# Optimization experiments

Hardware: AMD Instinct MI355X
Metric: run time of the kernel (lower is better)

The kernel has to match this reference:

```python
import jax, jax.numpy as jnp
import numpy as np

SEQ, BATCH, IN_DIM, HID_DIM = 512, 256, 256, 256
NQ = 8
ALPHA = 0.5
MLP_HID = 128


def _linear_init(key, fan_in, fan_out):
    k1, k2 = jax.random.split(key)
    bound = 1.0 / np.sqrt(fan_in)
    W = jax.random.uniform(k1, (fan_in, fan_out), minval=-bound, maxval=bound, dtype=jnp.float32)
    b = jax.random.uniform(k2, (fan_out,), minval=-bound, maxval=bound, dtype=jnp.float32)
    return W, b


def setup_inputs() -> dict:
    key = jax.random.key(0)
    ks = jax.random.split(key, 12)
    cdim = IN_DIM + HID_DIM
    inputs = jax.random.normal(ks[0], (SEQ, BATCH, IN_DIM), dtype=jnp.float32)
    W1, b1 = _linear_init(ks[1], cdim, MLP_HID)
    W2, b2 = _linear_init(ks[2], MLP_HID, NQ * 4)
    Wf, bf = _linear_init(ks[3], cdim, 1)
    Wi, bi = _linear_init(ks[4], cdim, 1)
    Wg, bg = _linear_init(ks[5], cdim, 1)
    Wo, bo = _linear_init(ks[6], cdim, 1)
    rzf = jax.random.normal(ks[7], (NQ,), dtype=jnp.float32)
    rzi = jax.random.normal(ks[8], (NQ,), dtype=jnp.float32)
    rzg = jax.random.normal(ks[9], (NQ,), dtype=jnp.float32)
    rzo = jax.random.normal(ks[10], (NQ,), dtype=jnp.float32)
    return dict(inputs=inputs, W1=W1, b1=b1, W2=W2, b2=b2,
                Wf=Wf, bf=bf, Wi=Wi, bi=bi, Wg=Wg, bg=bg, Wo=Wo, bo=bo,
                rzf=rzf, rzi=rzi, rzg=rzg, rzo=rzo)


def _qgate(theta):
    # Analytic expectations of the RX/RZ/CNOT-chain circuit:
    # <Z_k> = prod_{j<=k} cos(theta_j); rz_params cancel in Z expectations.
    # Returns mean over wires, shape (batch, 1).
    return jnp.mean(jnp.cumprod(jnp.cos(theta), axis=-1), axis=-1, keepdims=True)


def reference(inputs, W1, b1, W2, b2, Wf, bf, Wi, bi, Wg, bg, Wo, bo, rzf, rzi, rzg, rzo):
    batch = inputs.shape[1]
    hx0 = jnp.zeros((batch, HID_DIM), dtype=inputs.dtype)
    cx0 = jnp.zeros((batch, HID_DIM), dtype=inputs.dtype)

    def step(carry, x):
        hx, cx = carry
        combined = jnp.concatenate([x, hx], axis=1)  # (B, in+hid)
        f_c = jax.nn.sigmoid(combined @ Wf + bf)
        i_c = jax.nn.sigmoid(combined @ Wi + bi)
        g_c = jnp.tanh(combined @ Wg + bg)
        o_c = jax.nn.sigmoid(combined @ Wo + bo)
        h1 = jax.nn.relu(combined @ W1 + b1)
        q = h1 @ W2 + b2  # (B, 4*NQ)
        q_f = _qgate(q[:, 0 * NQ:1 * NQ])
        q_i = _qgate(q[:, 1 * NQ:2 * NQ])
        q_g = _qgate(q[:, 2 * NQ:3 * NQ])
        q_o = _qgate(q[:, 3 * NQ:4 * NQ])
        f = (1 - ALPHA) * f_c + ALPHA * jax.nn.sigmoid(q_f)
        i = (1 - ALPHA) * i_c + ALPHA * jax.nn.sigmoid(q_i)
        g = (1 - ALPHA) * g_c + ALPHA * jnp.tanh(q_g)
        o = (1 - ALPHA) * o_c + ALPHA * jax.nn.sigmoid(q_o)
        cx_new = f * cx + i * g
        hx_new = o * jnp.tanh(cx_new)
        return (hx_new, cx_new), hx_new

    (hx, cx), outputs = jax.lax.scan(step, (hx0, cx0), inputs)
    return outputs, (hx, cx)
```

## Files before the change

### kernel.cpp

```cpp
#include <hip/hip_runtime.h>

#define SEQ 512
#define BATCH 256
#define INDIM 256
#define MLP 128
#define M_ROWS (SEQ * BATCH)
#define PRE_STRIDE 136
#define AUX_OFF ((size_t)M_ROWS * PRE_STRIDE)

__global__ __launch_bounds__(256) void prep_kernel(
    const float* __restrict__ W1,
    const float* __restrict__ Wf, const float* __restrict__ Wi,
    const float* __restrict__ Wg, const float* __restrict__ Wo,
    const float* __restrict__ bf, const float* __restrict__ bi,
    const float* __restrict__ bg, const float* __restrict__ bo,
    float* __restrict__ aux) {
  const int tid = threadIdx.x;
  if (tid < 128) {
    float s = 0.f;
    for (int k = 0; k < 256; ++k) s += W1[(size_t)(256 + k) * 128 + tid];
    aux[tid] = s;
  } else if (tid < 132) {
    const int g = tid - 128;
    const float* w = (g == 0) ? Wf : (g == 1) ? Wi : (g == 2) ? Wg : Wo;
    float s = 0.f;
    for (int k = 0; k < 256; ++k) s += w[256 + k];
    aux[128 + g] = s;
  } else if (tid < 136) {
    const int g = tid - 132;
    const float* bp = (g == 0) ? bf : (g == 1) ? bi : (g == 2) ? bg : bo;
    aux[132 + g] = bp[0];
  }
}

#define BK 16
#define LDX 132

__global__ __launch_bounds__(256) void gemm_kernel(
    const float* __restrict__ X,
    const float* __restrict__ W1,
    const float* __restrict__ b1p,
    const float* __restrict__ Wf, const float* __restrict__ Wi,
    const float* __restrict__ Wg, const float* __restrict__ Wo,
    const float* __restrict__ bfp, const float* __restrict__ bip,
    const float* __restrict__ bgp, const float* __restrict__ bop,
    float* __restrict__ PRE) {
  __shared__ __align__(16) float Xs[BK * LDX];
  __shared__ __align__(16) float Ws[BK * LDX];
  __shared__ float Wgs[BK * 4];

  const int tid = threadIdx.x;
  const int blk = blockIdx.x;
  const int tx = tid & 15, ty = tid >> 4;
  const int r_st = tid >> 1, kh = (tid & 1) * 8;
  const int wk = tid >> 4, wn = (tid & 15) * 8;
  const int r2 = tid >> 1, gp = (tid & 1) * 2;

  const size_t rowbase = (size_t)blk * 128;

  float acc[8][8] = {};
  float ga = 0.f, gb = 0.f;

  for (int kc = 0; kc < 256; kc += BK) {
    const float4 xa = *(const float4*)&X[(rowbase + r_st) * 256 + kc + kh];
    const float4 xb = *(const float4*)&X[(rowbase + r_st) * 256 + kc + kh + 4];
    const float4 wa = *(const float4*)&W1[(size_t)(kc + wk) * 128 + wn];
    const float4 wb = *(const float4*)&W1[(size_t)(kc + wk) * 128 + wn + 4];
    float wgv = 0.f;
    if (tid < 64) {
      const int kk = tid >> 2, g = tid & 3;
      const float* w = (g == 0) ? Wf : (g == 1) ? Wi : (g == 2) ? Wg : Wo;
      wgv = w[kc + kk];
    }
    __syncthreads();
    Xs[(kh + 0) * LDX + r_st] = xa.x;
    Xs[(kh + 1) * LDX + r_st] = xa.y;
    Xs[(kh + 2) * LDX + r_st] = xa.z;
    Xs[(kh + 3) * LDX + r_st] = xa.w;
    Xs[(kh + 4) * LDX + r_st] = xb.x;
    Xs[(kh + 5) * LDX + r_st] = xb.y;
    Xs[(kh + 6) * LDX + r_st] = xb.z;
    Xs[(kh + 7) * LDX + r_st] = xb.w;
    *(float4*)&Ws[wk * LDX + wn] = wa;
    *(float4*)&Ws[wk * LDX + wn + 4] = wb;
    if (tid < 64) Wgs[tid] = wgv;
    __syncthreads();

#pragma unroll
    for (int kk = 0; kk < BK; ++kk) {
      const float4 a0 = *(const float4*)&Xs[kk * LDX + ty * 8];
      const float4 a1 = *(const float4*)&Xs[kk * LDX + ty * 8 + 4];
      const float4 c0 = *(const float4*)&Ws[kk * LDX + tx * 8];
      const float4 c1 = *(const float4*)&Ws[kk * LDX + tx * 8 + 4];
      const float av[8] = {a0.x, a0.y, a0.z, a0.w, a1.x, a1.y, a1.z, a1.w};
      const float bv[8] = {c0.x, c0.y, c0.z, c0.w, c1.x, c1.y, c1.z, c1.w};
#pragma unroll
      for (int i = 0; i < 8; ++i)
#pragma unroll
        for (int j = 0; j < 8; ++j)
          acc[i][j] = fmaf(av[i], bv[j], acc[i][j]);
      const float xv = Xs[kk * LDX + r2];
      ga = fmaf(xv, Wgs[kk * 4 + gp], ga);
      gb = fmaf(xv, Wgs[kk * 4 + gp + 1], gb);
    }
  }

  float bias[8];
  {
    const float4 u0 = *(const float4*)&b1p[tx * 8];
    const float4 u1 = *(const float4*)&b1p[tx * 8 + 4];
    bias[0] = u0.x; bias[1] = u0.y; bias[2] = u0.z; bias[3] = u0.w;
    bias[4] = u1.x; bias[5] = u1.y; bias[6] = u1.z; bias[7] = u1.w;
  }
#pragma unroll
  for (int i = 0; i < 8; ++i) {
    const size_t row = rowbase + ty * 8 + i;
    float4 o0, o1;
    o0.x = acc[i][0] + bias[0]; o0.y = acc[i][1] + bias[1];
    o0.z = acc[i][2] + bias[2]; o0.w = acc[i][3] + bias[3];
    o1.x = acc[i][4] + bias[4]; o1.y = acc[i][5] + bias[5];
    o1.z = acc[i][6] + bias[6]; o1.w = acc[i][7] + bias[7];
    *(float4*)&PRE[row * PRE_STRIDE + tx * 8] = o0;
    *(float4*)&PRE[row * PRE_STRIDE + tx * 8 + 4] = o1;
  }
  {
    const float ab = (gp == 0) ? bfp[0] : bgp[0];
    const float bb2 = (gp == 0) ? bip[0] : bop[0];
    float2 og;
    og.x = ga + ab; og.y = gb + bb2;
    *(float2*)&PRE[(rowbase + r2) * PRE_STRIDE + 128 + gp] = og;
  }
}

__device__ __forceinline__ float sigmoid_f(float x) {
  return __fdividef(1.0f, 1.0f + __expf(-x));
}
__device__ __forceinline__ float tanh_f(float x) {
  const float e = __expf(-2.0f * x);
  return __fdividef(1.0f - e, 1.0f + e);
}
__device__ __forceinline__ float readlane_f(float v, int lane) {
  return __int_as_float(__builtin_amdgcn_readlane(__float_as_int(v), lane));
}

__global__ __attribute__((amdgpu_waves_per_eu(1, 1))) __launch_bounds__(64)
void rec_kernel(
    const float* __restrict__ PRE, const float* __restrict__ W2,
    const float* __restrict__ b2, const float* __restrict__ aux,
    float* __restrict__ out) {
  __shared__ __align__(16) float h1s[128];

  const int l = threadIdx.x;
  const int b = blockIdx.x;
  const int m = l & 31, half = l >> 5;
  const int g = m >> 3;
  const int g8 = g * 8;

  float w2r[64];
#pragma unroll
  for (int u = 0; u < 64; ++u) w2r[u] = W2[(size_t)(half * 64 + u) * 32 + m];
  const float4 b2a = *(const float4*)&b2[g8];
  const float4 b2b = *(const float4*)&b2[g8 + 4];
  const float2 s1 = *(const float2*)&aux[2 * l];
  const float4 sg = *(const float4*)&aux[128];

  float h = 0.f, c = 0.f;

  const float* pr0 = PRE + (size_t)b * PRE_STRIDE;
  const size_t ts = (size_t)BATCH * PRE_STRIDE;

  float2 p0 = *(const float2*)(pr0 + 0 * ts + 2 * l);
  float4 g0 = *(const float4*)(pr0 + 0 * ts + 128);
  float2 p1 = *(const float2*)(pr0 + 1 * ts + 2 * l);
  float4 g1 = *(const float4*)(pr0 + 1 * ts + 128);

  const float4* h1p = (const float4*)&h1s[half * 64];

  for (int t = 0; t < SEQ; ++t) {
    const float h10 = fmaxf(fmaf(h, s1.x, p0.x), 0.f);
    const float h11 = fmaxf(fmaf(h, s1.y, p0.y), 0.f);

    ((float2*)h1s)[l] = make_float2(h10, h11);
    asm volatile("" ::: "memory");

    const float zf = fmaf(h, sg.x, g0.x);
    const float zi = fmaf(h, sg.y, g0.y);
    const float zg = fmaf(h, sg.z, g0.z);
    const float zo = fmaf(h, sg.w, g0.w);
    const float cf = sigmoid_f(zf);
    const float ci = sigmoid_f(zi);
    const float cg = tanh_f(zg);
    const float co = sigmoid_f(zo);
    p0 = p1; g0 = g1;
    const int tn = (t + 2 < SEQ) ? (t + 2) : (SEQ - 1);
    p1 = *(const float2*)(pr0 + (size_t)tn * ts + 2 * l);
    g1 = *(const float4*)(pr0 + (size_t)tn * ts + 128);

    float q0 = 0.f, q1 = 0.f, q2 = 0.f, q3 = 0.f;
#pragma unroll
    for (int jj = 0; jj < 16; ++jj) {
      const float4 hv = h1p[jj];
      q0 = fmaf(hv.x, w2r[4 * jj + 0], q0);
      q1 = fmaf(hv.y, w2r[4 * jj + 1], q1);
      q2 = fmaf(hv.z, w2r[4 * jj + 2], q2);
      q3 = fmaf(hv.w, w2r[4 * jj + 3], q3);
    }
    const float part = (q0 + q1) + (q2 + q3);

    const float a0 = __shfl(part, g8 + 0, 64), b0 = __shfl(part, 32 + g8 + 0, 64);
    const float a1 = __shfl(part, g8 + 1, 64), b1 = __shfl(part, 32 + g8 + 1, 64);
    const float a2 = __shfl(part, g8 + 2, 64), b2s = __shfl(part, 32 + g8 + 2, 64);
    const float a3 = __shfl(part, g8 + 3, 64), b3 = __shfl(part, 32 + g8 + 3, 64);
    const float a4 = __shfl(part, g8 + 4, 64), b4 = __shfl(part, 32 + g8 + 4, 64);
    const float a5 = __shfl(part, g8 + 5, 64), b5 = __shfl(part, 32 + g8 + 5, 64);
    const float a6 = __shfl(part, g8 + 6, 64), b6 = __shfl(part, 32 + g8 + 6, 64);
    const float a7 = __shfl(part, g8 + 7, 64), b7 = __shfl(part, 32 + g8 + 7, 64);

    const float e0 = __cosf(a0 + b0 + b2a.x);
    const float e1 = __cosf(a1 + b1 + b2a.y);
    const float e2 = __cosf(a2 + b2s + b2a.z);
    const float e3 = __cosf(a3 + b3 + b2a.w);
    const float e4 = __cosf(a4 + b4 + b2b.x);
    const float e5 = __cosf(a5 + b5 + b2b.y);
    const float e6 = __cosf(a6 + b6 + b2b.z);
    const float e7 = __cosf(a7 + b7 + b2b.w);
    float p = e0, s = e0;
    p *= e1; s += p;
    p *= e2; s += p;
    p *= e3; s += p;
    p *= e4; s += p;
    p *= e5; s += p;
    p *= e6; s += p;
    p *= e7; s += p;
    const float qv = s * 0.125f;

    const float qarg = (g == 2) ? (2.0f * qv) : qv;
    const float qs = sigmoid_f(qarg);
    const float av = (g == 2) ? (2.0f * qs - 1.0f) : qs;

    const float aF = readlane_f(av, 0);
    const float aI = readlane_f(av, 8);
    const float aG = readlane_f(av, 16);
    const float aO = readlane_f(av, 24);

    const float f  = 0.5f * (cf + aF);
    const float ii = 0.5f * (ci + aI);
    const float gg = 0.5f * (cg + aG);
    const float oo = 0.5f * (co + aO);

    c = fmaf(f, c, ii * gg);
    h = oo * tanh_f(c);

    float4 hv4o; hv4o.x = h; hv4o.y = h; hv4o.z = h; hv4o.w = h;
    *(float4*)(out + ((size_t)t * BATCH + b) * 256 + 4 * l) = hv4o;
  }

  float4 hq; hq.x = h; hq.y = h; hq.z = h; hq.w = h;
  float4 cq; cq.x = c; cq.y = c; cq.z = c; cq.w = c;
  *(float4*)(out + (size_t)SEQ * BATCH * 256 + (size_t)b * 256 + 4 * l) = hq;
  *(float4*)(out + (size_t)SEQ * BATCH * 256 + (size_t)BATCH * 256 +
             (size_t)b * 256 + 4 * l) = cq;
}

extern "C" void kernel_launch(void* const* d_in, const int* in_sizes, int n_in,
                              void* d_out, int out_size, void* d_ws,
                              size_t ws_size, hipStream_t stream) {
  const float* X  = (const float*)d_in[0];
  const float* W1 = (const float*)d_in[1];
  const float* b1 = (const float*)d_in[2];
  const float* W2 = (const float*)d_in[3];
  const float* b2 = (const float*)d_in[4];
  const float* Wf = (const float*)d_in[5];
  const float* bf = (const float*)d_in[6];
  const float* Wi = (const float*)d_in[7];
  const float* bi = (const float*)d_in[8];
  const float* Wg = (const float*)d_in[9];
  const float* bg = (const float*)d_in[10];
  const float* Wo = (const float*)d_in[11];
  const float* bo = (const float*)d_in[12];

  float* ws  = (float*)d_ws;
  float* PRE = ws;
  float* aux = ws + AUX_OFF;
  float* out = (float*)d_out;

  prep_kernel<<<1, 256, 0, stream>>>(W1, Wf, Wi, Wg, Wo, bf, bi, bg, bo, aux);
  gemm_kernel<<<M_ROWS / 128, 256, 0, stream>>>(X, W1, b1, Wf, Wi, Wg, Wo,
                                                bf, bi, bg, bo, PRE);
  rec_kernel<<<BATCH, 64, 0, stream>>>(PRE, W2, b2, aux, out);
}
```

Baseline: 755.4 us.

## Stage PRE rows via async global-to-LDS loads and streamline the q reduction

Each timestep's precomputed row is now fetched with global_load_lds into an 8-slot LDS ring, four steps ahead, with explicit vmcnt waits. Registers no longer carry the prefetch. The ReLU hidden activations are computed inside the W2 dot loop from LDS-held PRE and s1 values, which removes the h1 store to shared memory. The cross-half reduction is now a single xor shuffle, and each lane evaluates one cosine before shuffling, instead of 16 shuffles followed by 8 cosines. The risks are wrong manual vmcnt accounting, since the output stores also count toward vmcnt, and possible LDS layout or bank conflicts, traded against a shorter serial dependency chain per step.

```diff
diff --git a/kernel.cpp b/kernel.cpp
--- a/kernel.cpp
+++ b/kernel.cpp
@@ -143,12 +143,22 @@
   return __int_as_float(__builtin_amdgcn_readlane(__float_as_int(v), lane));
 }
 
+#define GLOBAL_AS __attribute__((address_space(1)))
+#define LDS_AS __attribute__((address_space(3)))
+
+__device__ __forceinline__ void stage_row16(const float* grow, float* lslot,
+                                            int lane) {
+  __builtin_amdgcn_global_load_lds((const GLOBAL_AS void*)(grow + 4 * lane),
+                                   (LDS_AS void*)lslot, 16, 0, 0);
+}
+
 __global__ __attribute__((amdgpu_waves_per_eu(1, 1))) __launch_bounds__(64)
 void rec_kernel(
     const float* __restrict__ PRE, const float* __restrict__ W2,
     const float* __restrict__ b2, const float* __restrict__ aux,
     float* __restrict__ out) {
-  __shared__ __align__(16) float h1s[128];
+  __shared__ __align__(16) float pstage[8 * 256];
+  __shared__ __align__(16) float s1s[128];
 
   const int l = threadIdx.x;
   const int b = blockIdx.x;
@@ -159,71 +169,74 @@
   float w2r[64];
 #pragma unroll
   for (int u = 0; u < 64; ++u) w2r[u] = W2[(size_t)(half * 64 + u) * 32 + m];
-  const float4 b2a = *(const float4*)&b2[g8];
-  const float4 b2b = *(const float4*)&b2[g8 + 4];
-  const float2 s1 = *(const float2*)&aux[2 * l];
+  const float b2m = b2[m];
   const float4 sg = *(const float4*)&aux[128];
 
-  float h = 0.f, c = 0.f;
+  *(float2*)&s1s[2 * l] = *(const float2*)&aux[2 * l];
 
   const float* pr0 = PRE + (size_t)b * PRE_STRIDE;
   const size_t ts = (size_t)BATCH * PRE_STRIDE;
 
-  float2 p0 = *(const float2*)(pr0 + 0 * ts + 2 * l);
-  float4 g0 = *(const float4*)(pr0 + 0 * ts + 128);
-  float2 p1 = *(const float2*)(pr0 + 1 * ts + 2 * l);
-  float4 g1 = *(const float4*)(pr0 + 1 * ts + 128);
-
-  const float4* h1p = (const float4*)&h1s[half * 64];
+#pragma unroll
+  for (int k = 0; k < 4; ++k)
+    stage_row16(pr0 + (size_t)k * ts, &pstage[k * 256], l);
+
+  float h = 0.f, c = 0.f;
 
   for (int t = 0; t < SEQ; ++t) {
-    const float h10 = fmaxf(fmaf(h, s1.x, p0.x), 0.f);
-    const float h11 = fmaxf(fmaf(h, s1.y, p0.y), 0.f);
-
-    ((float2*)h1s)[l] = make_float2(h10, h11);
-    asm volatile("" ::: "memory");
-
-    const float zf = fmaf(h, sg.x, g0.x);
-    const float zi = fmaf(h, sg.y, g0.y);
-    const float zg = fmaf(h, sg.z, g0.z);
-    const float zo = fmaf(h, sg.w, g0.w);
+    if (t < 4) {
+      asm volatile("s_waitcnt vmcnt(0)" ::: "memory");
+    } else {
+      asm volatile("s_waitcnt vmcnt(7)" ::: "memory");
+    }
+    __builtin_amdgcn_sched_barrier(0);
+
+    {
+      const int tn = (t + 4 < SEQ) ? (t + 4) : (SEQ - 1);
+      stage_row16(pr0 + (size_t)tn * ts, &pstage[((t + 4) & 7) * 256], l);
+    }
+
+    const float* slot = &pstage[(t & 7) * 256];
+
+    const float4 gpre = *(const float4*)&slot[128];
+    const float zf = fmaf(h, sg.x, gpre.x);
+    const float zi = fmaf(h, sg.y, gpre.y);
+    const float zg = fmaf(h, sg.z, gpre.z);
+    const float zo = fmaf(h, sg.w, gpre.w);
     const float cf = sigmoid_f(zf);
     const float ci = sigmoid_f(zi);
     const float cg = tanh_f(zg);
     const float co = sigmoid_f(zo);
-    p0 = p1; g0 = g1;
-    const int tn = (t + 2 < SEQ) ? (t + 2) : (SEQ - 1);
-    p1 = *(const float2*)(pr0 + (size_t)tn * ts + 2 * l);
-    g1 = *(const float4*)(pr0 + (size_t)tn * ts + 128);
-
+
+    const float* ps = slot + half * 64;
+    const float* ss = s1s + half * 64;
     float q0 = 0.f, q1 = 0.f, q2 = 0.f, q3 = 0.f;
 #pragma unroll
-    for (int jj = 0; jj < 16; ++jj) {
-      const float4 hv = h1p[jj];
-      q0 = fmaf(hv.x, w2r[4 * jj + 0], q0);
-      q1 = fmaf(hv.y, w2r[4 * jj + 1], q1);
-      q2 = fmaf(hv.z, w2r[4 * jj + 2], q2);
-      q3 = fmaf(hv.w, w2r[4 * jj + 3], q3);
-    }
-    const float part = (q0 + q1) + (q2 + q3);
-
-    const float a0 = __shfl(part, g8 + 0, 64), b0 = __shfl(part, 32 + g8 + 0, 64);
-    const float a1 = __shfl(part, g8 + 1, 64), b1 = __shfl(part, 32 + g8 + 1, 64);
-    const float a2 = __shfl(part, g8 + 2, 64), b2s = __shfl(part, 32 + g8 + 2, 64);
-    const float a3 = __shfl(part, g8 + 3, 64), b3 = __shfl(part, 32 + g8 + 3, 64);
-    const float a4 = __shfl(part, g8 + 4, 64), b4 = __shfl(part, 32 + g8 + 4, 64);
-    const float a5 = __shfl(part, g8 + 5, 64), b5 = __shfl(part, 32 + g8 + 5, 64);
-    const float a6 = __shfl(part, g8 + 6, 64), b6 = __shfl(part, 32 + g8 + 6, 64);
-    const float a7 = __shfl(part, g8 + 7, 64), b7 = __shfl(part, 32 + g8 + 7, 64);
-
-    const float e0 = __cosf(a0 + b0 + b2a.x);
-    const float e1 = __cosf(a1 + b1 + b2a.y);
-    const float e2 = __cosf(a2 + b2s + b2a.z);
-    const float e3 = __cosf(a3 + b3 + b2a.w);
-    const float e4 = __cosf(a4 + b4 + b2b.x);
-    const float e5 = __cosf(a5 + b5 + b2b.y);
-    const float e6 = __cosf(a6 + b6 + b2b.z);
-    const float e7 = __cosf(a7 + b7 + b2b.w);
+    for (int j = 0; j < 16; ++j) {
+      const float4 pv = *(const float4*)&ps[4 * j];
+      const float4 sv = *(const float4*)&ss[4 * j];
+      const float x0 = fmaxf(fmaf(h, sv.x, pv.x), 0.f);
+      const float x1 = fmaxf(fmaf(h, sv.y, pv.y), 0.f);
+      const float x2 = fmaxf(fmaf(h, sv.z, pv.z), 0.f);
+      const float x3 = fmaxf(fmaf(h, sv.w, pv.w), 0.f);
+      q0 = fmaf(x0, w2r[4 * j + 0], q0);
+      q1 = fmaf(x1, w2r[4 * j + 1], q1);
+      q2 = fmaf(x2, w2r[4 * j + 2], q2);
+      q3 = fmaf(x3, w2r[4 * j + 3], q3);
+    }
+    float part = (q0 + q1) + (q2 + q3);
+    part += __shfl_xor(part, 32, 64);
+
+    const float cm = __cosf(part + b2m);
+    const int sb = (l & 32) + g8;
+    const float e0 = __shfl(cm, sb + 0, 64);
+    const float e1 = __shfl(cm, sb + 1, 64);
+    const float e2 = __shfl(cm, sb + 2, 64);
+    const float e3 = __shfl(cm, sb + 3, 64);
+    const float e4 = __shfl(cm, sb + 4, 64);
+    const float e5 = __shfl(cm, sb + 5, 64);
+    const float e6 = __shfl(cm, sb + 6, 64);
+    const float e7 = __shfl(cm, sb + 7, 64);
     float p = e0, s = e0;
     p *= e1; s += p;
     p *= e2; s += p;
@@ -251,8 +264,8 @@
     c = fmaf(f, c, ii * gg);
     h = oo * tanh_f(c);
 
-    float4 hv4o; hv4o.x = h; hv4o.y = h; hv4o.z = h; hv4o.w = h;
-    *(float4*)(out + ((size_t)t * BATCH + b) * 256 + 4 * l) = hv4o;
+    float4 hv4; hv4.x = h; hv4.y = h; hv4.z = h; hv4.w = h;
+    *(float4*)(out + ((size_t)t * BATCH + b) * 256 + 4 * l) = hv4;
   }
 
   float4 hq; hq.x = h; hq.y = h; hq.z = h; hq.w = h;
```

Result: slower. 984.6 us (+30.3%).

## Fuse GEMM and recurrence into one kernel with per-timestep flag synchronization

Applied to the files above, without the earlier changes.

Merges the input-projection GEMM and the sequential recurrence into a single launch. The first 256 blocks run the recurrence, and the remaining blocks compute PRE tiles and publish per-tile completion flags. Recurrence blocks spin on the flag for timestep t+2 before prefetching, so the serial recurrence can start while the GEMM is still running instead of waiting for the whole GEMM. The risks are that recurrence blocks now use 256-thread launches with most lanes idle, that spinning and atomics add overhead, and that correctness depends on all blocks being resident, with a bounded spin guard as fallback.

```diff
diff --git a/kernel.cpp b/kernel.cpp
--- a/kernel.cpp
+++ b/kernel.cpp
@@ -7,6 +7,12 @@
 #define M_ROWS (SEQ * BATCH)
 #define PRE_STRIDE 136
 #define AUX_OFF ((size_t)M_ROWS * PRE_STRIDE)
+
+#define NBLK_REC 256
+#define NBLK_GEMM (M_ROWS / 128)
+
+__device__ unsigned g_epoch;
+__device__ unsigned g_flags[NBLK_GEMM];
 
 __global__ __launch_bounds__(256) void prep_kernel(
     const float* __restrict__ W1,
@@ -31,12 +37,35 @@
     const float* bp = (g == 0) ? bf : (g == 1) ? bi : (g == 2) ? bg : bo;
     aux[132 + g] = bp[0];
   }
+  if (tid == 0)
+    __hip_atomic_fetch_add(&g_epoch, 1u, __ATOMIC_RELAXED,
+                           __HIP_MEMORY_SCOPE_AGENT);
 }
 
 #define BK 16
 #define LDX 132
 
-__global__ __launch_bounds__(256) void gemm_kernel(
+__device__ __forceinline__ float sigmoid_f(float x) {
+  return __fdividef(1.0f, 1.0f + __expf(-x));
+}
+__device__ __forceinline__ float tanh_f(float x) {
+  const float e = __expf(-2.0f * x);
+  return __fdividef(1.0f - e, 1.0f + e);
+}
+__device__ __forceinline__ float readlane_f(float v, int lane) {
+  return __int_as_float(__builtin_amdgcn_readlane(__float_as_int(v), lane));
+}
+
+__device__ __forceinline__ void spin_flag(const unsigned* fp, unsigned target) {
+  int guard = 0;
+  while (__hip_atomic_load(fp, __ATOMIC_ACQUIRE, __HIP_MEMORY_SCOPE_AGENT) <
+         target) {
+    __builtin_amdgcn_s_sleep(2);
+    if (++guard > (1 << 19)) break;
+  }
+}
+
+__global__ __launch_bounds__(256) void fused_kernel(
     const float* __restrict__ X,
     const float* __restrict__ W1,
     const float* __restrict__ b1p,
@@ -44,113 +73,111 @@
     const float* __restrict__ Wg, const float* __restrict__ Wo,
     const float* __restrict__ bfp, const float* __restrict__ bip,
     const float* __restrict__ bgp, const float* __restrict__ bop,
-    float* __restrict__ PRE) {
-  __shared__ __align__(16) float Xs[BK * LDX];
-  __shared__ __align__(16) float Ws[BK * LDX];
-  __shared__ float Wgs[BK * 4];
-
-  const int tid = threadIdx.x;
-  const int blk = blockIdx.x;
-  const int tx = tid & 15, ty = tid >> 4;
-  const int r_st = tid >> 1, kh = (tid & 1) * 8;
-  const int wk = tid >> 4, wn = (tid & 15) * 8;
-  const int r2 = tid >> 1, gp = (tid & 1) * 2;
-
-  const size_t rowbase = (size_t)blk * 128;
-
-  float acc[8][8] = {};
-  float ga = 0.f, gb = 0.f;
-
-  for (int kc = 0; kc < 256; kc += BK) {
-    const float4 xa = *(const float4*)&X[(rowbase + r_st) * 256 + kc + kh];
-    const float4 xb = *(const float4*)&X[(rowbase + r_st) * 256 + kc + kh + 4];
-    const float4 wa = *(const float4*)&W1[(size_t)(kc + wk) * 128 + wn];
-    const float4 wb = *(const float4*)&W1[(size_t)(kc + wk) * 128 + wn + 4];
-    float wgv = 0.f;
-    if (tid < 64) {
-      const int kk = tid >> 2, g = tid & 3;
-      const float* w = (g == 0) ? Wf : (g == 1) ? Wi : (g == 2) ? Wg : Wo;
-      wgv = w[kc + kk];
-    }
+    const float* __restrict__ W2, const float* __restrict__ b2,
+    const float* __restrict__ aux,
+    float* __restrict__ PRE, float* __restrict__ out) {
+  __shared__ __align__(16) float lds[BK * LDX * 2 + BK * 4];
+
+  if (blockIdx.x >= NBLK_REC) {
+    float* Xs = lds;
+    float* Ws = lds + BK * LDX;
+    float* Wgs = lds + 2 * BK * LDX;
+
+    const int tid = threadIdx.x;
+    const int gblk = blockIdx.x - NBLK_REC;
+    const int tx = tid & 15, ty = tid >> 4;
+    const int r_st = tid >> 1, kh = (tid & 1) * 8;
+    const int wk = tid >> 4, wn = (tid & 15) * 8;
+    const int r2 = tid >> 1, gp = (tid & 1) * 2;
+
+    const size_t rowbase = (size_t)gblk * 128;
+
+    float acc[8][8] = {};
+    float ga = 0.f, gb = 0.f;
+
+    for (int kc = 0; kc < 256; kc += BK) {
+      const float4 xa = *(const float4*)&X[(rowbase + r_st) * 256 + kc + kh];
+      const float4 xb = *(const float4*)&X[(rowbase + r_st) * 256 + kc + kh + 4];
+      const float4 wa = *(const float4*)&W1[(size_t)(kc + wk) * 128 + wn];
+      const float4 wb = *(const float4*)&W1[(size_t)(kc + wk) * 128 + wn + 4];
+      float wgv = 0.f;
+      if (tid < 64) {
+        const int kk = tid >> 2, g = tid & 3;
+        const float* w = (g == 0) ? Wf : (g == 1) ? Wi : (g == 2) ? Wg : Wo;
+        wgv = w[kc + kk];
+      }
+      __syncthreads();
+      Xs[(kh + 0) * LDX + r_st] = xa.x;
+      Xs[(kh + 1) * LDX + r_st] = xa.y;
+      Xs[(kh + 2) * LDX + r_st] = xa.z;
+      Xs[(kh + 3) * LDX + r_st] = xa.w;
+      Xs[(kh + 4) * LDX + r_st] = xb.x;
+      Xs[(kh + 5) * LDX + r_st] = xb.y;
+      Xs[(kh + 6) * LDX + r_st] = xb.z;
+      Xs[(kh + 7) * LDX + r_st] = xb.w;
+      *(float4*)&Ws[wk * LDX + wn] = wa;
+      *(float4*)&Ws[wk * LDX + wn + 4] = wb;
+      if (tid < 64) Wgs[tid] = wgv;
+      __syncthreads();
+
+#pragma unroll
+      for (int kk = 0; kk < BK; ++kk) {
+        const float4 a0 = *(const float4*)&Xs[kk * LDX + ty * 8];
+        const float4 a1 = *(const float4*)&Xs[kk * LDX + ty * 8 + 4];
+        const float4 c0 = *(const float4*)&Ws[kk * LDX + tx * 8];
+        const float4 c1 = *(const float4*)&Ws[kk * LDX + tx * 8 + 4];
+        const float av[8] = {a0.x, a0.y, a0.z, a0.w, a1.x, a1.y, a1.z, a1.w};
+        const float bv[8] = {c0.x, c0.y, c0.z, c0.w, c1.x, c1.y, c1.z, c1.w};
+#pragma unroll
+        for (int i = 0; i < 8; ++i)
+#pragma unroll
+          for (int j = 0; j < 8; ++j)
+            acc[i][j] = fmaf(av[i], bv[j], acc[i][j]);
+        const float xv = Xs[kk * LDX + r2];
+        ga = fmaf(xv, Wgs[kk * 4 + gp], ga);
+        gb = fmaf(xv, Wgs[kk * 4 + gp + 1], gb);
+      }
+    }
+
+    float bias[8];
+    {
+      const float4 u0 = *(const float4*)&b1p[tx * 8];
+      const float4 u1 = *(const float4*)&b1p[tx * 8 + 4];
+      bias[0] = u0.x; bias[1] = u0.y; bias[2] = u0.z; bias[3] = u0.w;
+      bias[4] = u1.x; bias[5] = u1.y; bias[6] = u1.z; bias[7] = u1.w;
+    }
+#pragma unroll
+    for (int i = 0; i < 8; ++i) {
+      const size_t row = rowbase + ty * 8 + i;
+      float4 o0, o1;
+      o0.x = acc[i][0] + bias[0]; o0.y = acc[i][1] + bias[1];
+      o0.z = acc[i][2] + bias[2]; o0.w = acc[i][3] + bias[3];
+      o1.x = acc[i][4] + bias[4]; o1.y = acc[i][5] + bias[5];
+      o1.z = acc[i][6] + bias[6]; o1.w = acc[i][7] + bias[7];
+      *(float4*)&PRE[row * PRE_STRIDE + tx * 8] = o0;
+      *(float4*)&PRE[row * PRE_STRIDE + tx * 8 + 4] = o1;
+    }
+    {
+      const float ab = (gp == 0) ? bfp[0] : bgp[0];
+      const float bb2 = (gp == 0) ? bip[0] : bop[0];
+      float2 og;
+      og.x = ga + ab; og.y = gb + bb2;
+      *(float2*)&PRE[(rowbase + r2) * PRE_STRIDE + 128 + gp] = og;
+    }
+
     __syncthreads();
-    Xs[(kh + 0) * LDX + r_st] = xa.x;
-    Xs[(kh + 1) * LDX + r_st] = xa.y;
-    Xs[(kh + 2) * LDX + r_st] = xa.z;
-    Xs[(kh + 3) * LDX + r_st] = xa.w;
-    Xs[(kh + 4) * LDX + r_st] = xb.x;
-    Xs[(kh + 5) * LDX + r_st] = xb.y;
-    Xs[(kh + 6) * LDX + r_st] = xb.z;
-    Xs[(kh + 7) * LDX + r_st] = xb.w;
-    *(float4*)&Ws[wk * LDX + wn] = wa;
-    *(float4*)&Ws[wk * LDX + wn + 4] = wb;
-    if (tid < 64) Wgs[tid] = wgv;
-    __syncthreads();
-
-#pragma unroll
-    for (int kk = 0; kk < BK; ++kk) {
-      const float4 a0 = *(const float4*)&Xs[kk * LDX + ty * 8];
-      const float4 a1 = *(const float4*)&Xs[kk * LDX + ty * 8 + 4];
-      const float4 c0 = *(const float4*)&Ws[kk * LDX + tx * 8];
-      const float4 c1 = *(const float4*)&Ws[kk * LDX + tx * 8 + 4];
-      const float av[8] = {a0.x, a0.y, a0.z, a0.w, a1.x, a1.y, a1.z, a1.w};
-      const float bv[8] = {c0.x, c0.y, c0.z, c0.w, c1.x, c1.y, c1.z, c1.w};
-#pragma unroll
-      for (int i = 0; i < 8; ++i)
-#pragma unroll
-        for (int j = 0; j < 8; ++j)
-          acc[i][j] = fmaf(av[i], bv[j], acc[i][j]);
-      const float xv = Xs[kk * LDX + r2];
-      ga = fmaf(xv, Wgs[kk * 4 + gp], ga);
-      gb = fmaf(xv, Wgs[kk * 4 + gp + 1], gb);
-    }
+    if (tid == 0) {
+      __threadfence();
+      __hip_atomic_fetch_add(&g_flags[gblk], 1u, __ATOMIC_RELEASE,
+                             __HIP_MEMORY_SCOPE_AGENT);
+    }
+    return;
   }
 
-  float bias[8];
-  {
-    const float4 u0 = *(const float4*)&b1p[tx * 8];
-    const float4 u1 = *(const float4*)&b1p[tx * 8 + 4];
-    bias[0] = u0.x; bias[1] = u0.y; bias[2] = u0.z; bias[3] = u0.w;
-    bias[4] = u1.x; bias[5] = u1.y; bias[6] = u1.z; bias[7] = u1.w;
-  }
-#pragma unroll
-  for (int i = 0; i < 8; ++i) {
-    const size_t row = rowbase + ty * 8 + i;
-    float4 o0, o1;
-    o0.x = acc[i][0] + bias[0]; o0.y = acc[i][1] + bias[1];
-    o0.z = acc[i][2] + bias[2]; o0.w = acc[i][3] + bias[3];
-    o1.x = acc[i][4] + bias[4]; o1.y = acc[i][5] + bias[5];
-    o1.z = acc[i][6] + bias[6]; o1.w = acc[i][7] + bias[7];
-    *(float4*)&PRE[row * PRE_STRIDE + tx * 8] = o0;
-    *(float4*)&PRE[row * PRE_STRIDE + tx * 8 + 4] = o1;
-  }
-  {
-    const float ab = (gp == 0) ? bfp[0] : bgp[0];
-    const float bb2 = (gp == 0) ? bip[0] : bop[0];
-    float2 og;
-    og.x = ga + ab; og.y = gb + bb2;
-    *(float2*)&PRE[(rowbase + r2) * PRE_STRIDE + 128 + gp] = og;
-  }
-}
-
-__device__ __forceinline__ float sigmoid_f(float x) {
-  return __fdividef(1.0f, 1.0f + __expf(-x));
-}
-__device__ __forceinline__ float tanh_f(float x) {
-  const float e = __expf(-2.0f * x);
-  return __fdividef(1.0f - e, 1.0f + e);
-}
-__device__ __forceinline__ float readlane_f(float v, int lane) {
-  return __int_as_float(__builtin_amdgcn_readlane(__float_as_int(v), lane));
-}
-
-__global__ __attribute__((amdgpu_waves_per_eu(1, 1))) __launch_bounds__(64)
-void rec_kernel(
-    const float* __restrict__ PRE, const float* __restrict__ W2,
-    const float* __restrict__ b2, const float* __restrict__ aux,
-    float* __restrict__ out) {
-  __shared__ __align__(16) float h1s[128];
-
   const int l = threadIdx.x;
+  if (l >= 64) return;
+  float* h1s = lds;
+
   const int b = blockIdx.x;
   const int m = l & 31, half = l >> 5;
   const int g = m >> 3;
@@ -164,6 +191,13 @@
   const float2 s1 = *(const float2*)&aux[2 * l];
   const float4 sg = *(const float4*)&aux[128];
 
+  const unsigned target =
+      __hip_atomic_load(&g_epoch, __ATOMIC_RELAXED, __HIP_MEMORY_SCOPE_AGENT);
+  const int hb = (b >= 128) ? 1 : 0;
+
+  spin_flag(&g_flags[0 + hb], target);
+  spin_flag(&g_flags[2 + hb], target);
+
   float h = 0.f, c = 0.f;
 
   const float* pr0 = PRE + (size_t)b * PRE_STRIDE;
@@ -177,6 +211,10 @@
   const float4* h1p = (const float4*)&h1s[half * 64];
 
   for (int t = 0; t < SEQ; ++t) {
+    const int tn = (t + 2 < SEQ) ? (t + 2) : (SEQ - 1);
+    const unsigned fv = __hip_atomic_load(
+        &g_flags[2 * tn + hb], __ATOMIC_ACQUIRE, __HIP_MEMORY_SCOPE_AGENT);
+
     const float h10 = fmaxf(fmaf(h, s1.x, p0.x), 0.f);
     const float h11 = fmaxf(fmaf(h, s1.y, p0.y), 0.f);
 
@@ -191,8 +229,10 @@
     const float ci = sigmoid_f(zi);
     const float cg = tanh_f(zg);
     const float co = sigmoid_f(zo);
+
+    if (fv < target) spin_flag(&g_flags[2 * tn + hb], target);
+
     p0 = p1; g0 = g1;
-    const int tn = (t + 2 < SEQ) ? (t + 2) : (SEQ - 1);
     p1 = *(const float2*)(pr0 + (size_t)tn * ts + 2 * l);
     g1 = *(const float4*)(pr0 + (size_t)tn * ts + 128);
 
@@ -285,7 +325,6 @@
   float* out = (float*)d_out;
 
   prep_kernel<<<1, 256, 0, stream>>>(W1, Wf, Wi, Wg, Wo, bf, bi, bg, bo, aux);
-  gemm_kernel<<<M_ROWS / 128, 256, 0, stream>>>(X, W1, b1, Wf, Wi, Wg, Wo,
-                                                bf, bi, bg, bo, PRE);
-  rec_kernel<<<BATCH, 64, 0, stream>>>(PRE, W2, b2, aux, out);
-}
+  fused_kernel<<<NBLK_REC + NBLK_GEMM, 256, 0, stream>>>(
+      X, W1, b1, Wf, Wi, Wg, Wo, bf, bi, bg, bo, W2, b2, aux, PRE, out);
+}
```

New measurement: 1.419 ms. 87.9% more time.
